# Optimization experiments

Hardware: AMD Instinct MI355X
Metric: run time of the kernel (lower is better)

## Reference

```python
import jax, jax.numpy as jnp
import numpy as np

B, C, DD, HH, WW = 1, 128, 16, 16, 16
D_STATE, D_CONV, EXPAND = 16, 4, 2
D_INNER = EXPAND * C
DT_RANK = (C + 15) // 16


def setup_inputs():
    key = jax.random.key(0)
    ks = jax.random.split(key, 10)
    def w(k, shape, s=0.02):
        return jax.random.normal(k, shape, dtype=jnp.float32) * s
    return {
        "x": jax.random.normal(ks[0], (B, C, DD, HH, WW), dtype=jnp.float32),
        "ln_w": jnp.ones((C,), jnp.float32),
        "ln_b": jnp.zeros((C,), jnp.float32),
        "mnorm_w": jnp.ones((C,), jnp.float32),
        "mnorm_b": jnp.zeros((C,), jnp.float32),
        "in_proj_w": w(ks[1], (2 * D_INNER, C)),
        "conv_w": w(ks[2], (D_INNER, D_CONV), 0.2),
        "conv_b": jnp.zeros((D_INNER,), jnp.float32),
        "x_proj_w": w(ks[3], (DT_RANK + 2 * D_STATE, D_INNER)),
        "dt_proj_w": w(ks[4], (D_INNER, DT_RANK), 0.1),
        "dt_proj_b": jnp.full((D_INNER,), float(np.log(np.expm1(0.01))), jnp.float32),
        "A_log": jnp.log(jnp.tile(jnp.arange(1, D_STATE + 1, dtype=jnp.float32), (D_INNER, 1))),
        "D_param": jnp.ones((D_INNER,), jnp.float32),
        "out_proj_w": w(ks[5], (C, D_INNER)),
        "proj_w": w(ks[6], (C, 3 * C)),
        "proj_b": jnp.zeros((C,), jnp.float32),
        "fc1_w": w(ks[7], (4 * C, C)),
        "fc1_b": jnp.zeros((4 * C,), jnp.float32),
        "fc2_w": w(ks[8], (C, 4 * C)),
        "fc2_b": jnp.zeros((C,), jnp.float32),
    }


def _ln_cf(x, w, b, eps=1e-6):
    # channels_first LayerNorm over axis 1 (matches custom LayerNorm)
    u = x.mean(1, keepdims=True)
    s = ((x - u) ** 2).mean(1, keepdims=True)
    xn = (x - u) * jax.lax.rsqrt(s + eps)
    return w[None, :, None, None, None] * xn + b[None, :, None, None, None]


def _ln_last(x, w, b, eps=1e-5):
    u = x.mean(-1, keepdims=True)
    s = ((x - u) ** 2).mean(-1, keepdims=True)
    return (x - u) * jax.lax.rsqrt(s + eps) * w + b


def _selective_scan(u, delta, A, Bm, Cm, Dv):
    # u, delta: (N,L,d); Bm,Cm: (N,L,n); A: (d,n); Dv: (d,)
    dA = jnp.exp(delta[..., None] * A)                               # (N,L,d,n)
    dBu = delta[..., None] * Bm[:, :, None, :] * u[..., None]         # (N,L,d,n)
    def step(h, inp):
        dA_t, dBu_t, C_t = inp
        h = dA_t * h + dBu_t
        y = jnp.einsum("bdn,bn->bd", h, C_t)
        return h, y
    h0 = jnp.zeros((u.shape[0], A.shape[0], A.shape[1]), u.dtype)
    _, ys = jax.lax.scan(step, h0, (dA.swapaxes(0, 1), dBu.swapaxes(0, 1), Cm.swapaxes(0, 1)))
    return ys.swapaxes(0, 1) + u * Dv


def _mamba(xin, in_proj_w, conv_w, conv_b, x_proj_w, dt_proj_w, dt_proj_b, A_log, D_param, out_proj_w):
    # xin: (N, L, C)
    N, L, _ = xin.shape
    xz = xin @ in_proj_w.T                                            # (N,L,2*d_inner)
    xr, z = jnp.split(xz, 2, axis=-1)
    # causal depthwise conv1d, kernel D_CONV, left-padded (mamba conv1d[..., :L])
    xp = jnp.pad(xr, ((0, 0), (D_CONV - 1, 0), (0, 0)))
    xc = sum(conv_w[:, k] * xp[:, k:k + L, :] for k in range(D_CONV)) + conv_b
    xc = jax.nn.silu(xc)
    x_dbl = xc @ x_proj_w.T                                           # (N,L,dt_rank+2n)
    dt = x_dbl[..., :DT_RANK]
    Bm = x_dbl[..., DT_RANK:DT_RANK + D_STATE]
    Cm = x_dbl[..., DT_RANK + D_STATE:]
    delta = jax.nn.softplus(dt @ dt_proj_w.T + dt_proj_b)
    A = -jnp.exp(A_log)
    y = _selective_scan(xc, delta, A, Bm, Cm, D_param)
    y = y * jax.nn.silu(z)
    return y @ out_proj_w.T


def _forward(x, ln_w, ln_b, mnorm_w, mnorm_b, in_proj_w, conv_w, conv_b, x_proj_w, dt_proj_w, dt_proj_b, A_log, D_param, out_proj_w, proj_w, proj_b, fc1_w, fc1_b, fc2_w, fc2_b):
    Bb, Cc, Dd, Hh, Ww = x.shape
    L = Dd * Hh * Ww
    x1 = _ln_cf(x, ln_w, ln_b)
    # three directional flattenings (d-, h-, w-major); cube => shapes identical
    xd = x1.reshape(Bb, Cc, L)
    xh = x1.transpose(0, 1, 3, 4, 2).reshape(Bb, Cc, L)
    xw = x1.transpose(0, 1, 4, 2, 3).reshape(Bb, Cc, L)
    seq = jnp.stack([xd, xh, xw], 0).reshape(3 * Bb, Cc, L).swapaxes(1, 2)  # (3B,L,C)
    seq = _ln_last(seq, mnorm_w, mnorm_b)
    y = _mamba(seq, in_proj_w, conv_w, conv_b, x_proj_w, dt_proj_w, dt_proj_b, A_log, D_param, out_proj_w)
    # reassemble per-direction volumes (no inverse permute, matching torch code) and concat on channels
    cat = y.swapaxes(1, 2).reshape(3, Bb, Cc, Dd, Hh, Ww).transpose(1, 0, 2, 3, 4, 5).reshape(Bb, 3 * Cc, Dd, Hh, Ww)
    out1 = jnp.einsum("bkdhw,ok->bodhw", cat, proj_w) + proj_b[None, :, None, None, None]
    out_res = x + out1
    h = _ln_cf(out_res, ln_w, ln_b)
    h = jnp.einsum("bcdhw,oc->bodhw", h, fc1_w) + fc1_b[None, :, None, None, None]
    h = jax.nn.gelu(h, approximate=False)
    h = jnp.einsum("bcdhw,oc->bodhw", h, fc2_w) + fc2_b[None, :, None, None, None]
    return h + out_res


def reference(x, ln_w, ln_b, mnorm_w, mnorm_b, in_proj_w, conv_w, conv_b, x_proj_w, dt_proj_w, dt_proj_b, A_log, D_param, out_proj_w, proj_w, proj_b, fc1_w, fc1_b, fc2_w, fc2_b):
    return _forward(x, ln_w, ln_b, mnorm_w, mnorm_b, in_proj_w, conv_w, conv_b, x_proj_w, dt_proj_w, dt_proj_b, A_log, D_param, out_proj_w, proj_w, proj_b, fc1_w, fc1_b, fc2_w, fc2_b)
```

## Files before the change

### kernel.cpp

```cpp
#include <hip/hip_runtime.h>
#include <hip/hip_bf16.h>
#include <math.h>

#define L 4096
#define C 128
#define DI 256
#define NST 16
#define NS 3
#define NCH 256
#define CT 16
#define R3 12288

__device__ __forceinline__ float siluf(float x){ return x / (1.f + __expf(-x)); }
__device__ __forceinline__ float geluf(float x){ return 0.5f*x*(1.f + erff(x*0.70710678118654752f)); }

__device__ __forceinline__ int permf(int s, int l){
  if(s==0) return l;
  if(s==1) return ((l&15)<<8) | ((l>>8)<<4) | ((l>>4)&15);
  return (((l>>4)&15)<<8) | ((l&15)<<4) | (l>>8);
}

__global__ void k_M(const float* __restrict__ opw, const float* __restrict__ pw,
                    float* __restrict__ Mw){
  int b = blockIdx.x;
  int o = b & 127, s = b >> 7;
  int d = threadIdx.x;
  float acc = 0.f;
  for(int c=0;c<C;c++) acc += opw[c*DI + d] * pw[o*384 + s*128 + c];
  Mw[(s*256+d)*128 + o] = acc;
}

__global__ void k_lngemm(const float* __restrict__ x, const float* __restrict__ lw,
                         const float* __restrict__ lb, const float* __restrict__ mw,
                         const float* __restrict__ mb, const float* __restrict__ ipw,
                         float* __restrict__ Z){
  __shared__ float As[128][68];
  __shared__ float Bs[64][132];
  int p0 = blockIdx.x*64, j0 = blockIdx.y*64;
  int tid = threadIdx.x;
  for(int q=0;q<8;q++){
    int f = q*1024 + tid*4; int cc = f>>6, p = f&63;
    float4 v = *(const float4*)&x[cc*L + p0 + p];
    *(float4*)&As[cc][p] = v;
  }
  for(int q=0;q<8;q++){
    int f = q*1024 + tid*4; int j = f>>7, k = f&127;
    float4 b = *(const float4*)&ipw[(j0+j)*C + k];
    *(float4*)&Bs[j][k] = b;
  }
  __syncthreads();
  {
    int p = tid>>2, kg = tid&3;
    float s=0.f, sq=0.f;
    #pragma unroll
    for(int i=0;i<32;i++){
      int k = kg*32 + ((i + kg*2)&31);
      float v = As[k][p]; s += v; sq += v*v;
    }
    s  += __shfl_xor(s,1);  s  += __shfl_xor(s,2);
    sq += __shfl_xor(sq,1); sq += __shfl_xor(sq,2);
    float m1 = s*(1.f/C);
    float r1 = rsqrtf(sq*(1.f/C) - m1*m1 + 1e-6f);
    float s2=0.f, sq2=0.f;
    #pragma unroll
    for(int i=0;i<32;i++){
      int k = kg*32 + ((i + kg*2)&31);
      float t = lw[k]*((As[k][p]-m1)*r1) + lb[k];
      s2 += t; sq2 += t*t;
    }
    s2  += __shfl_xor(s2,1);  s2  += __shfl_xor(s2,2);
    sq2 += __shfl_xor(sq2,1); sq2 += __shfl_xor(sq2,2);
    float m2 = s2*(1.f/C);
    float r2 = rsqrtf(sq2*(1.f/C) - m2*m2 + 1e-5f);
    #pragma unroll
    for(int i=0;i<32;i++){
      int k = kg*32 + ((i + kg*2)&31);
      float t = lw[k]*((As[k][p]-m1)*r1) + lb[k];
      As[k][p] = mw[k]*((t-m2)*r2) + mb[k];
    }
  }
  __syncthreads();
  int og = tid & 15, r4 = tid >> 4;
  float acc[4][4] = {};
  for(int k=0;k<128;k++){
    float4 av = *(const float4*)&As[k][r4*4];
    float a[4] = {av.x, av.y, av.z, av.w};
    float b[4];
    #pragma unroll
    for(int j=0;j<4;j++) b[j] = Bs[og+16*j][k];
    #pragma unroll
    for(int i=0;i<4;i++)
      #pragma unroll
      for(int j=0;j<4;j++) acc[i][j] += a[i]*b[j];
  }
  #pragma unroll
  for(int i=0;i<4;i++)
    #pragma unroll
    for(int j=0;j<4;j++)
      Z[(p0+r4*4+i)*512 + j0 + og + 16*j] = acc[i][j];
}

__global__ void k_conv(const float* __restrict__ Z, const float* __restrict__ cw,
                       const float* __restrict__ cb, float* __restrict__ xc){
  int bl = blockIdx.x;
  int s = bl >> 12, l = bl & 4095;
  int d = threadIdx.x;
  float acc = cb[d];
  #pragma unroll
  for(int k=0;k<4;k++){
    int lk = l - 3 + k;
    if(lk >= 0){
      int p = permf(s, lk);
      acc += cw[d*4+k] * Z[p*512 + d];
    }
  }
  xc[bl*DI + d] = siluf(acc);
}

__global__ void k_xd4a(const float* __restrict__ xc, const float* __restrict__ xpw,
                       float* __restrict__ xp){
  __shared__ float As[32][132];
  __shared__ float Ws[40][132];
  int r0 = blockIdx.x*32;
  int k0 = blockIdx.y*128;
  int tid = threadIdx.x;
  for(int q=0;q<4;q++){
    int f = q*256 + tid; int r = f>>5, kk = (f&31)*4;
    float4 v = *(const float4*)&xc[(r0+r)*DI + k0 + kk];
    *(float4*)&As[r][kk] = v;
  }
  for(int q=0;q<5;q++){
    int f = q*256 + tid; int col = f>>5, kk = (f&31)*4;
    float4 v = *(const float4*)&xpw[col*DI + k0 + kk];
    *(float4*)&Ws[col][kk] = v;
  }
  __syncthreads();
  int r = tid & 31, cg = tid >> 5;
  float acc[5] = {0.f,0.f,0.f,0.f,0.f};
  for(int k4=0;k4<32;k4++){
    float4 a = *(const float4*)&As[r][k4*4];
    #pragma unroll
    for(int j=0;j<5;j++){
      float4 w = *(const float4*)&Ws[cg*5+j][k4*4];
      acc[j] += a.x*w.x + a.y*w.y + a.z*w.z + a.w*w.w;
    }
  }
  float* dst = xp + (blockIdx.y*12288 + r0 + r)*40 + cg*5;
  #pragma unroll
  for(int j=0;j<5;j++) dst[j] = acc[j];
}

__global__ void k_xd4b(const float* __restrict__ xp, const float* __restrict__ dtw,
                       const float* __restrict__ dtb, float* __restrict__ Bc,
                       float* __restrict__ Cc, float* __restrict__ delta){
  __shared__ float xdb[40][17];
  int r0 = blockIdx.x*16;
  int tid = threadIdx.x;
  for(int e=tid; e<640; e+=256){
    int row = e/40, col = e%40;
    int idx = (r0+row)*40 + col;
    xdb[col][row] = xp[idx] + xp[491520 + idx];
  }
  __syncthreads();
  {
    float4 ww0 = *(const float4*)&dtw[tid*8];
    float4 ww1 = *(const float4*)&dtw[tid*8+4];
    float bb = dtb[tid];
    #pragma unroll 4
    for(int r=0;r<16;r++){
      float aa = bb + xdb[0][r]*ww0.x + xdb[1][r]*ww0.y + xdb[2][r]*ww0.z + xdb[3][r]*ww0.w
                    + xdb[4][r]*ww1.x + xdb[5][r]*ww1.y + xdb[6][r]*ww1.z + xdb[7][r]*ww1.w;
      delta[(r0+r)*DI + tid] = (aa > 20.f) ? aa : log1pf(__expf(aa));
    }
  }
  if(tid < 64){
    int rr = tid>>2, ng = (tid&3)*4;
    float4 bv = make_float4(xdb[8+ng][rr], xdb[9+ng][rr], xdb[10+ng][rr], xdb[11+ng][rr]);
    *(float4*)&Bc[(r0+rr)*NST + ng] = bv;
  } else if(tid < 128){
    int t2 = tid - 64;
    int rr = t2>>2, ng = (t2&3)*4;
    float4 cv = make_float4(xdb[24+ng][rr], xdb[25+ng][rr], xdb[26+ng][rr], xdb[27+ng][rr]);
    *(float4*)&Cc[(r0+rr)*NST + ng] = cv;
  }
}

__global__ void k_scanA(const float* __restrict__ delta, const float* __restrict__ xc,
                        const float* __restrict__ Bc, const float* __restrict__ A_log,
                        float* __restrict__ aggA, float* __restrict__ aggB){
  int b = blockIdx.x;
  int ng = b & 3, ch = (b>>2)&255, s = b>>10;
  int d = threadIdx.x;
  int n0 = ng*4;
  float Aa[4], P[4] = {1.f,1.f,1.f,1.f}, S[4] = {0.f,0.f,0.f,0.f};
  #pragma unroll
  for(int j=0;j<4;j++) Aa[j] = -__expf(A_log[d*NST + n0 + j]);
  int base = s*L + ch*CT;
  #pragma unroll
  for(int st=0; st<CT; st++){
    int row = base + st;
    float dl = delta[row*DI + d];
    float u  = xc[row*DI + d];
    float4 bv = *(const float4*)&Bc[row*NST + n0];
    float dlu = dl*u;
    float a;
    a = __expf(dl*Aa[0]); S[0] = a*S[0] + dlu*bv.x; P[0] *= a;
    a = __expf(dl*Aa[1]); S[1] = a*S[1] + dlu*bv.y; P[1] *= a;
    a = __expf(dl*Aa[2]); S[2] = a*S[2] + dlu*bv.z; P[2] *= a;
    a = __expf(dl*Aa[3]); S[3] = a*S[3] + dlu*bv.w; P[3] *= a;
  }
  int idx0 = ch*R3 + s*256 + d;
  #pragma unroll
  for(int j=0;j<4;j++){
    int idx = idx0 + (n0+j)*768;
    aggA[idx] = P[j]; aggB[idx] = S[j];
  }
}

__global__ void k_scanB(const float* __restrict__ aggA, const float* __restrict__ aggB,
                        float* __restrict__ hIn){
  __shared__ float PA[32][9], PB[32][9];
  int tid = threadIdx.x;
  int jl = tid & 31, seg = tid >> 5;
  int j = blockIdx.x*32 + jl;
  int c0 = seg*32;
  float pa[32], pb[32];
  float P = 1.f, S = 0.f;
  #pragma unroll
  for(int i=0;i<32;i++){
    pa[i] = P; pb[i] = S;
    float a = aggA[(c0+i)*R3 + j], b = aggB[(c0+i)*R3 + j];
    S = a*S + b; P = a*P;
  }
  PA[jl][seg] = P; PB[jl][seg] = S;
  __syncthreads();
  if(tid < 32){
    float h = 0.f;
    #pragma unroll
    for(int sg=0; sg<8; sg++){
      float p = PA[tid][sg], s2 = PB[tid][sg];
      PA[tid][sg] = h;
      h = p*h + s2;
    }
  }
  __syncthreads();
  float h0 = PA[jl][seg];
  #pragma unroll
  for(int i=0;i<32;i++){
    hIn[(c0+i)*R3 + j] = pa[i]*h0 + pb[i];
  }
}

__global__ void k_scanC(const float* __restrict__ delta, const float* __restrict__ xc,
                        const float* __restrict__ Bc, const float* __restrict__ Cc,
                        const float* __restrict__ A_log, const float* __restrict__ Dp,
                        const float* __restrict__ Z, const float* __restrict__ hIn,
                        float* __restrict__ yz){
  int b = blockIdx.x;
  int ch = b & 255, s = b >> 8;
  int d = threadIdx.x;
  float Aa[16], h[16];
  #pragma unroll
  for(int n=0;n<16;n++) Aa[n] = -__expf(A_log[d*NST + n]);
  #pragma unroll
  for(int n=0;n<16;n++) h[n] = hIn[ch*R3 + n*768 + s*256 + d];
  float Dv = Dp[d];
  int base = s*L + ch*CT;
  #pragma unroll 2
  for(int st=0; st<CT; st++){
    int row = base + st;
    float dl = delta[row*DI + d];
    float u  = xc[row*DI + d];
    float dlu = dl*u;
    const float4* Bp = (const float4*)&Bc[row*NST];
    const float4* Cp = (const float4*)&Cc[row*NST];
    float y = u*Dv;
    #pragma unroll
    for(int q=0;q<4;q++){
      float4 bv = Bp[q], cv = Cp[q];
      float a;
      a = __expf(dl*Aa[4*q+0]); h[4*q+0] = a*h[4*q+0] + dlu*bv.x; y += h[4*q+0]*cv.x;
      a = __expf(dl*Aa[4*q+1]); h[4*q+1] = a*h[4*q+1] + dlu*bv.y; y += h[4*q+1]*cv.y;
      a = __expf(dl*Aa[4*q+2]); h[4*q+2] = a*h[4*q+2] + dlu*bv.z; y += h[4*q+2]*cv.z;
      a = __expf(dl*Aa[4*q+3]); h[4*q+3] = a*h[4*q+3] + dlu*bv.w; y += h[4*q+3]*cv.w;
    }
    int l = ch*CT + st;
    int p = permf(s, l);
    float zv = Z[p*512 + 256 + d];
    yz[(s*L + l)*DI + d] = y * siluf(zv);
  }
}

__global__ void k_proj(const float* __restrict__ yz, const float* __restrict__ Mw,
                       float* __restrict__ pp){
  __shared__ float As[64][68];
  __shared__ float Bs[64][132];
  int p0 = blockIdx.x*64; int kc = blockIdx.y;
  int s = kc >> 1, d0 = (kc & 1)*128;
  int tid = threadIdx.x;
  int og = tid & 15, r4 = tid >> 4;
  float acc[4][8] = {};
  for(int kk=0; kk<2; kk++){
    int kb = d0 + kk*64;
    for(int q=0;q<4;q++){
      int f = q*1024 + tid*4; int r = f>>6, k = f&63;
      float4 a = *(const float4*)&yz[(s*L + p0 + r)*DI + kb + k];
      *(float4*)&As[r][k] = a;
    }
    for(int q=0;q<8;q++){
      int f = q*1024 + tid*4; int k = f>>7, o = f&127;
      float4 b = *(const float4*)&Mw[(s*256 + kb + k)*128 + o];
      *(float4*)&Bs[k][o] = b;
    }
    __syncthreads();
    for(int k=0;k<64;k++){
      float a[4];
      #pragma unroll
      for(int i=0;i<4;i++) a[i] = As[r4*4+i][k];
      #pragma unroll
      for(int j=0;j<8;j++){
        float bb = Bs[k][og+16*j];
        #pragma unroll
        for(int i=0;i<4;i++) acc[i][j] += a[i]*bb;
      }
    }
    __syncthreads();
  }
  float* dst = pp + kc*524288;
  #pragma unroll
  for(int i=0;i<4;i++)
    #pragma unroll
    for(int j=0;j<8;j++)
      dst[(p0+r4*4+i)*C + og + 16*j] = acc[i][j];
}

__global__ void k_pred(const float* __restrict__ pp, const float* __restrict__ x,
                       const float* __restrict__ pb, float* __restrict__ ores){
  __shared__ float Xs[16][129];
  int p0 = blockIdx.x*16; int tid = threadIdx.x;
  for(int q=0;q<8;q++){
    int f = q*256 + tid; int pl = f&15, o = f>>4;
    Xs[pl][o] = x[o*L + p0 + pl];
  }
  __syncthreads();
  for(int q=0;q<8;q++){
    int f = q*256 + tid; int o = f&127, pl = f>>7;
    int idx = (p0+pl)*C + o;
    float v = pp[idx] + pp[524288+idx] + pp[1048576+idx]
            + pp[1572864+idx] + pp[2097152+idx] + pp[2621440+idx];
    ores[idx] = v + Xs[pl][o] + pb[o];
  }
}

__global__ void k_fc1(const float* __restrict__ ores, const float* __restrict__ lw,
                      const float* __restrict__ lb, const float* __restrict__ w1,
                      const float* __restrict__ b1, float* __restrict__ H){
  __shared__ float As[64][129];
  __shared__ float Bs[64][129];
  int p0 = blockIdx.x*64, j0 = blockIdx.y*64;
  int tid = threadIdx.x;
  for(int q=0;q<8;q++){
    int f = q*1024 + tid*4; int r = f>>7, k = f&127;
    float4 a = *(const float4*)&ores[(p0+r)*C + k];
    As[r][k]=a.x; As[r][k+1]=a.y; As[r][k+2]=a.z; As[r][k+3]=a.w;
    float4 b = *(const float4*)&w1[(j0+r)*C + k];
    Bs[r][k]=b.x; Bs[r][k+1]=b.y; Bs[r][k+2]=b.z; Bs[r][k+3]=b.w;
  }
  __syncthreads();
  {
    int r = tid>>2, kg = tid&3;
    float s=0.f, sq=0.f;
    #pragma unroll
    for(int i=0;i<32;i++){
      int k = kg*32 + ((i + kg*8)&31);
      float v = As[r][k]; s += v; sq += v*v;
    }
    s  += __shfl_xor(s,1);  s  += __shfl_xor(s,2);
    sq += __shfl_xor(sq,1); sq += __shfl_xor(sq,2);
    float m1 = s*(1.f/C);
    float r1 = rsqrtf(sq*(1.f/C) - m1*m1 + 1e-6f);
    #pragma unroll
    for(int i=0;i<32;i++){
      int k = kg*32 + ((i + kg*8)&31);
      As[r][k] = lw[k]*((As[r][k]-m1)*r1) + lb[k];
    }
  }
  __syncthreads();
  int og = tid & 15, r4 = tid >> 4;
  float acc[4][4] = {};
  for(int k=0;k<128;k++){
    float a[4], b[4];
    #pragma unroll
    for(int i=0;i<4;i++) a[i] = As[r4*4+i][k];
    #pragma unroll
    for(int j=0;j<4;j++) b[j] = Bs[og+16*j][k];
    #pragma unroll
    for(int i=0;i<4;i++)
      #pragma unroll
      for(int j=0;j<4;j++) acc[i][j] += a[i]*b[j];
  }
  #pragma unroll
  for(int i=0;i<4;i++)
    #pragma unroll
    for(int j=0;j<4;j++){
      int jj = j0 + og + 16*j;
      H[(p0+r4*4+i)*512 + jj] = geluf(acc[i][j] + b1[jj]);
    }
}

__global__ void k_fc2(const float* __restrict__ H, const float* __restrict__ w2,
                      float* __restrict__ fp){
  __shared__ float As[64][68];
  __shared__ float Bs[128][68];
  int p0 = blockIdx.x*64; int kc = blockIdx.y;
  int tid = threadIdx.x;
  int og = tid & 15, r4 = tid >> 4;
  float acc[4][8] = {};
  for(int kk=0; kk<2; kk++){
    int kb = kc*128 + kk*64;
    for(int q=0;q<4;q++){
      int f = q*1024 + tid*4; int r = f>>6, k = f&63;
      float4 a = *(const float4*)&H[(p0+r)*512 + kb + k];
      *(float4*)&As[r][k] = a;
    }
    for(int q=0;q<8;q++){
      int f = q*1024 + tid*4; int o = f>>6, k = f&63;
      float4 b = *(const float4*)&w2[o*512 + kb + k];
      *(float4*)&Bs[o][k] = b;
    }
    __syncthreads();
    for(int k=0;k<64;k++){
      float a[4];
      #pragma unroll
      for(int i=0;i<4;i++) a[i] = As[r4*4+i][k];
      #pragma unroll
      for(int j=0;j<8;j++){
        float bb = Bs[og+16*j][k];
        #pragma unroll
        for(int i=0;i<4;i++) acc[i][j] += a[i]*bb;
      }
    }
    __syncthreads();
  }
  float* dst = fp + kc*524288;
  #pragma unroll
  for(int i=0;i<4;i++)
    #pragma unroll
    for(int j=0;j<8;j++)
      dst[(p0+r4*4+i)*C + og + 16*j] = acc[i][j];
}

__global__ void k_fred(const float* __restrict__ fp, const float* __restrict__ b2,
                       const float* __restrict__ ores, float* __restrict__ out){
  __shared__ float S[128][17];
  int p0 = blockIdx.x*16; int tid = threadIdx.x;
  for(int q=0;q<8;q++){
    int f = q*256 + tid; int o = f&127, pl = f>>7;
    int idx = (p0+pl)*C + o;
    float v = fp[idx] + fp[524288+idx] + fp[1048576+idx] + fp[1572864+idx];
    S[o][pl] = v + b2[o] + ores[idx];
  }
  __syncthreads();
  for(int q=0;q<8;q++){
    int f = q*256 + tid; int pl = f&15, o = f>>4;
    out[o*L + p0 + pl] = S[o][pl];
  }
}

extern "C" void kernel_launch(void* const* d_in, const int* in_sizes, int n_in,
                              void* d_out, int out_size, void* d_ws, size_t ws_size,
                              hipStream_t stream) {
  const float* x     = (const float*)d_in[0];
  const float* ln_w  = (const float*)d_in[1];
  const float* ln_b  = (const float*)d_in[2];
  const float* mw    = (const float*)d_in[3];
  const float* mb    = (const float*)d_in[4];
  const float* ipw   = (const float*)d_in[5];
  const float* cw    = (const float*)d_in[6];
  const float* cb    = (const float*)d_in[7];
  const float* xpw   = (const float*)d_in[8];
  const float* dtw   = (const float*)d_in[9];
  const float* dtb   = (const float*)d_in[10];
  const float* A_log = (const float*)d_in[11];
  const float* Dp    = (const float*)d_in[12];
  const float* opw   = (const float*)d_in[13];
  const float* pw    = (const float*)d_in[14];
  const float* pb    = (const float*)d_in[15];
  const float* w1    = (const float*)d_in[16];
  const float* b1    = (const float*)d_in[17];
  const float* w2    = (const float*)d_in[18];
  const float* b2    = (const float*)d_in[19];
  float* out = (float*)d_out;

  float* ws = (float*)d_ws;
  float* Z     = ws;
  float* xc    = Z     + 2097152;
  float* delta = xc    + 3145728;
  float* dt    = delta + 3145728;
  float* Bc    = dt    + 98304;
  float* Cc    = Bc    + 196608;
  float* aggA  = Cc    + 196608;
  float* aggB  = aggA  + 3145728;
  float* hIn   = aggB  + 3145728;
  float* Mw    = hIn   + 3145728;
  float* ores  = Mw    + 98304;
  (void)dt;
  float* xp = hIn;
  float* yz = aggA;
  float* pp = delta;
  float* H  = Z;
  float* fp = xc;

  k_M     <<<384, 256, 0, stream>>>(opw, pw, Mw);
  k_lngemm<<<dim3(64,8), 256, 0, stream>>>(x, ln_w, ln_b, mw, mb, ipw, Z);
  k_conv  <<<NS*L, 256, 0, stream>>>(Z, cw, cb, xc);
  k_xd4a  <<<dim3(384,2), 256, 0, stream>>>(xc, xpw, xp);
  k_xd4b  <<<768, 256, 0, stream>>>(xp, dtw, dtb, Bc, Cc, delta);
  k_scanA <<<3072, 256, 0, stream>>>(delta, xc, Bc, A_log, aggA, aggB);
  k_scanB <<<384, 256, 0, stream>>>(aggA, aggB, hIn);
  k_scanC <<<768, 256, 0, stream>>>(delta, xc, Bc, Cc, A_log, Dp, Z, hIn, yz);
  k_proj  <<<dim3(64,6), 256, 0, stream>>>(yz, Mw, pp);
  k_pred  <<<256, 256, 0, stream>>>(pp, x, pb, ores);
  k_fc1   <<<dim3(64,8), 256, 0, stream>>>(ores, ln_w, ln_b, w1, b1, H);
  k_fc2   <<<dim3(64,4), 256, 0, stream>>>(H, w2, fp);
  k_fred  <<<256, 256, 0, stream>>>(fp, b2, ores, out);
}
```

Baseline: 274.3 us.

## Store large intermediate activations in bf16 to halve memory traffic

Converts the big workspace intermediates (Z, xc, delta, scan aggregates, hidden states, yz, partial projection sums, fc1 output, fc2 partials) from fp32 to bf16 storage, with fp32 arithmetic inside kernels. Conversions are round-to-nearest-even bit manipulations, and the workspace layout is rebuilt with byte offsets. This targets the memory-bound pipeline of thirteen kernels, where most time is spent moving these tensors. It costs precision, especially in the scan aggregates and hidden-state carries, which can compound error across the sequence.

```diff
diff --git a/kernel.cpp b/kernel.cpp
--- a/kernel.cpp
+++ b/kernel.cpp
@@ -11,8 +11,20 @@
 #define CT 16
 #define R3 12288
 
+typedef unsigned short u16;
+
 __device__ __forceinline__ float siluf(float x){ return x / (1.f + __expf(-x)); }
 __device__ __forceinline__ float geluf(float x){ return 0.5f*x*(1.f + erff(x*0.70710678118654752f)); }
+
+__device__ __forceinline__ float b2f(u16 h){ return __uint_as_float(((unsigned)h)<<16); }
+__device__ __forceinline__ u16 f2b(float f){
+  unsigned u = __float_as_uint(f);
+  return (u16)((u + 0x7FFFu + ((u>>16)&1u)) >> 16);
+}
+__device__ __forceinline__ float4 b4f(const u16* p){
+  ushort4 v = *(const ushort4*)p;
+  return make_float4(b2f(v.x), b2f(v.y), b2f(v.z), b2f(v.w));
+}
 
 __device__ __forceinline__ int permf(int s, int l){
   if(s==0) return l;
@@ -33,7 +45,7 @@
 __global__ void k_lngemm(const float* __restrict__ x, const float* __restrict__ lw,
                          const float* __restrict__ lb, const float* __restrict__ mw,
                          const float* __restrict__ mb, const float* __restrict__ ipw,
-                         float* __restrict__ Z){
+                         u16* __restrict__ Zb){
   __shared__ float As[128][68];
   __shared__ float Bs[64][132];
   int p0 = blockIdx.x*64, j0 = blockIdx.y*64;
@@ -97,11 +109,11 @@
   for(int i=0;i<4;i++)
     #pragma unroll
     for(int j=0;j<4;j++)
-      Z[(p0+r4*4+i)*512 + j0 + og + 16*j] = acc[i][j];
-}
-
-__global__ void k_conv(const float* __restrict__ Z, const float* __restrict__ cw,
-                       const float* __restrict__ cb, float* __restrict__ xc){
+      Zb[(p0+r4*4+i)*512 + j0 + og + 16*j] = f2b(acc[i][j]);
+}
+
+__global__ void k_conv(const u16* __restrict__ Zb, const float* __restrict__ cw,
+                       const float* __restrict__ cb, u16* __restrict__ xcb){
   int bl = blockIdx.x;
   int s = bl >> 12, l = bl & 4095;
   int d = threadIdx.x;
@@ -111,13 +123,13 @@
     int lk = l - 3 + k;
     if(lk >= 0){
       int p = permf(s, lk);
-      acc += cw[d*4+k] * Z[p*512 + d];
-    }
-  }
-  xc[bl*DI + d] = siluf(acc);
-}
-
-__global__ void k_xd4a(const float* __restrict__ xc, const float* __restrict__ xpw,
+      acc += cw[d*4+k] * b2f(Zb[p*512 + d]);
+    }
+  }
+  xcb[bl*DI + d] = f2b(siluf(acc));
+}
+
+__global__ void k_xd4a(const u16* __restrict__ xcb, const float* __restrict__ xpw,
                        float* __restrict__ xp){
   __shared__ float As[32][132];
   __shared__ float Ws[40][132];
@@ -126,7 +138,7 @@
   int tid = threadIdx.x;
   for(int q=0;q<4;q++){
     int f = q*256 + tid; int r = f>>5, kk = (f&31)*4;
-    float4 v = *(const float4*)&xc[(r0+r)*DI + k0 + kk];
+    float4 v = b4f(&xcb[(r0+r)*DI + k0 + kk]);
     *(float4*)&As[r][kk] = v;
   }
   for(int q=0;q<5;q++){
@@ -152,7 +164,7 @@
 
 __global__ void k_xd4b(const float* __restrict__ xp, const float* __restrict__ dtw,
                        const float* __restrict__ dtb, float* __restrict__ Bc,
-                       float* __restrict__ Cc, float* __restrict__ delta){
+                       float* __restrict__ Cc, u16* __restrict__ deltab){
   __shared__ float xdb[40][17];
   int r0 = blockIdx.x*16;
   int tid = threadIdx.x;
@@ -170,7 +182,8 @@
     for(int r=0;r<16;r++){
       float aa = bb + xdb[0][r]*ww0.x + xdb[1][r]*ww0.y + xdb[2][r]*ww0.z + xdb[3][r]*ww0.w
                     + xdb[4][r]*ww1.x + xdb[5][r]*ww1.y + xdb[6][r]*ww1.z + xdb[7][r]*ww1.w;
-      delta[(r0+r)*DI + tid] = (aa > 20.f) ? aa : log1pf(__expf(aa));
+      float dl = (aa > 20.f) ? aa : log1pf(__expf(aa));
+      deltab[(r0+r)*DI + tid] = f2b(dl);
     }
   }
   if(tid < 64){
@@ -185,9 +198,9 @@
   }
 }
 
-__global__ void k_scanA(const float* __restrict__ delta, const float* __restrict__ xc,
+__global__ void k_scanA(const u16* __restrict__ deltab, const u16* __restrict__ xcb,
                         const float* __restrict__ Bc, const float* __restrict__ A_log,
-                        float* __restrict__ aggA, float* __restrict__ aggB){
+                        u16* __restrict__ aggAb, u16* __restrict__ aggBb){
   int b = blockIdx.x;
   int ng = b & 3, ch = (b>>2)&255, s = b>>10;
   int d = threadIdx.x;
@@ -199,8 +212,8 @@
   #pragma unroll
   for(int st=0; st<CT; st++){
     int row = base + st;
-    float dl = delta[row*DI + d];
-    float u  = xc[row*DI + d];
+    float dl = b2f(deltab[row*DI + d]);
+    float u  = b2f(xcb[row*DI + d]);
     float4 bv = *(const float4*)&Bc[row*NST + n0];
     float dlu = dl*u;
     float a;
@@ -213,12 +226,12 @@
   #pragma unroll
   for(int j=0;j<4;j++){
     int idx = idx0 + (n0+j)*768;
-    aggA[idx] = P[j]; aggB[idx] = S[j];
-  }
-}
-
-__global__ void k_scanB(const float* __restrict__ aggA, const float* __restrict__ aggB,
-                        float* __restrict__ hIn){
+    aggAb[idx] = f2b(P[j]); aggBb[idx] = f2b(S[j]);
+  }
+}
+
+__global__ void k_scanB(const u16* __restrict__ aggAb, const u16* __restrict__ aggBb,
+                        u16* __restrict__ hInb){
   __shared__ float PA[32][9], PB[32][9];
   int tid = threadIdx.x;
   int jl = tid & 31, seg = tid >> 5;
@@ -229,7 +242,7 @@
   #pragma unroll
   for(int i=0;i<32;i++){
     pa[i] = P; pb[i] = S;
-    float a = aggA[(c0+i)*R3 + j], b = aggB[(c0+i)*R3 + j];
+    float a = b2f(aggAb[(c0+i)*R3 + j]), b = b2f(aggBb[(c0+i)*R3 + j]);
     S = a*S + b; P = a*P;
   }
   PA[jl][seg] = P; PB[jl][seg] = S;
@@ -247,15 +260,15 @@
   float h0 = PA[jl][seg];
   #pragma unroll
   for(int i=0;i<32;i++){
-    hIn[(c0+i)*R3 + j] = pa[i]*h0 + pb[i];
-  }
-}
-
-__global__ void k_scanC(const float* __restrict__ delta, const float* __restrict__ xc,
+    hInb[(c0+i)*R3 + j] = f2b(pa[i]*h0 + pb[i]);
+  }
+}
+
+__global__ void k_scanC(const u16* __restrict__ deltab, const u16* __restrict__ xcb,
                         const float* __restrict__ Bc, const float* __restrict__ Cc,
                         const float* __restrict__ A_log, const float* __restrict__ Dp,
-                        const float* __restrict__ Z, const float* __restrict__ hIn,
-                        float* __restrict__ yz){
+                        const u16* __restrict__ Zb, const u16* __restrict__ hInb,
+                        u16* __restrict__ yzb){
   int b = blockIdx.x;
   int ch = b & 255, s = b >> 8;
   int d = threadIdx.x;
@@ -263,14 +276,14 @@
   #pragma unroll
   for(int n=0;n<16;n++) Aa[n] = -__expf(A_log[d*NST + n]);
   #pragma unroll
-  for(int n=0;n<16;n++) h[n] = hIn[ch*R3 + n*768 + s*256 + d];
+  for(int n=0;n<16;n++) h[n] = b2f(hInb[ch*R3 + n*768 + s*256 + d]);
   float Dv = Dp[d];
   int base = s*L + ch*CT;
   #pragma unroll 2
   for(int st=0; st<CT; st++){
     int row = base + st;
-    float dl = delta[row*DI + d];
-    float u  = xc[row*DI + d];
+    float dl = b2f(deltab[row*DI + d]);
+    float u  = b2f(xcb[row*DI + d]);
     float dlu = dl*u;
     const float4* Bp = (const float4*)&Bc[row*NST];
     const float4* Cp = (const float4*)&Cc[row*NST];
@@ -286,13 +299,13 @@
     }
     int l = ch*CT + st;
     int p = permf(s, l);
-    float zv = Z[p*512 + 256 + d];
-    yz[(s*L + l)*DI + d] = y * siluf(zv);
-  }
-}
-
-__global__ void k_proj(const float* __restrict__ yz, const float* __restrict__ Mw,
-                       float* __restrict__ pp){
+    float zv = b2f(Zb[p*512 + 256 + d]);
+    yzb[(s*L + l)*DI + d] = f2b(y * siluf(zv));
+  }
+}
+
+__global__ void k_proj(const u16* __restrict__ yzb, const float* __restrict__ Mw,
+                       u16* __restrict__ ppb){
   __shared__ float As[64][68];
   __shared__ float Bs[64][132];
   int p0 = blockIdx.x*64; int kc = blockIdx.y;
@@ -303,8 +316,8 @@
   for(int kk=0; kk<2; kk++){
     int kb = d0 + kk*64;
     for(int q=0;q<4;q++){
-      int f = q*1024 + tid*4; int r = f>>6, k = f&63;
-      float4 a = *(const float4*)&yz[(s*L + p0 + r)*DI + kb + k];
+      int f = q*256 + tid; int r = f>>4, k = (f&15)*4;
+      float4 a = b4f(&yzb[(s*L + p0 + r)*DI + kb + k]);
       *(float4*)&As[r][k] = a;
     }
     for(int q=0;q<8;q++){
@@ -326,15 +339,15 @@
     }
     __syncthreads();
   }
-  float* dst = pp + kc*524288;
+  u16* dst = ppb + kc*524288;
   #pragma unroll
   for(int i=0;i<4;i++)
     #pragma unroll
     for(int j=0;j<8;j++)
-      dst[(p0+r4*4+i)*C + og + 16*j] = acc[i][j];
-}
-
-__global__ void k_pred(const float* __restrict__ pp, const float* __restrict__ x,
+      dst[(p0+r4*4+i)*C + og + 16*j] = f2b(acc[i][j]);
+}
+
+__global__ void k_pred(const u16* __restrict__ ppb, const float* __restrict__ x,
                        const float* __restrict__ pb, float* __restrict__ ores){
   __shared__ float Xs[16][129];
   int p0 = blockIdx.x*16; int tid = threadIdx.x;
@@ -346,15 +359,15 @@
   for(int q=0;q<8;q++){
     int f = q*256 + tid; int o = f&127, pl = f>>7;
     int idx = (p0+pl)*C + o;
-    float v = pp[idx] + pp[524288+idx] + pp[1048576+idx]
-            + pp[1572864+idx] + pp[2097152+idx] + pp[2621440+idx];
+    float v = b2f(ppb[idx]) + b2f(ppb[524288+idx]) + b2f(ppb[1048576+idx])
+            + b2f(ppb[1572864+idx]) + b2f(ppb[2097152+idx]) + b2f(ppb[2621440+idx]);
     ores[idx] = v + Xs[pl][o] + pb[o];
   }
 }
 
 __global__ void k_fc1(const float* __restrict__ ores, const float* __restrict__ lw,
                       const float* __restrict__ lb, const float* __restrict__ w1,
-                      const float* __restrict__ b1, float* __restrict__ H){
+                      const float* __restrict__ b1, u16* __restrict__ Hb){
   __shared__ float As[64][129];
   __shared__ float Bs[64][129];
   int p0 = blockIdx.x*64, j0 = blockIdx.y*64;
@@ -404,12 +417,12 @@
     #pragma unroll
     for(int j=0;j<4;j++){
       int jj = j0 + og + 16*j;
-      H[(p0+r4*4+i)*512 + jj] = geluf(acc[i][j] + b1[jj]);
-    }
-}
-
-__global__ void k_fc2(const float* __restrict__ H, const float* __restrict__ w2,
-                      float* __restrict__ fp){
+      Hb[(p0+r4*4+i)*512 + jj] = f2b(geluf(acc[i][j] + b1[jj]));
+    }
+}
+
+__global__ void k_fc2(const u16* __restrict__ Hb, const float* __restrict__ w2,
+                      u16* __restrict__ fpb){
   __shared__ float As[64][68];
   __shared__ float Bs[128][68];
   int p0 = blockIdx.x*64; int kc = blockIdx.y;
@@ -419,8 +432,8 @@
   for(int kk=0; kk<2; kk++){
     int kb = kc*128 + kk*64;
     for(int q=0;q<4;q++){
-      int f = q*1024 + tid*4; int r = f>>6, k = f&63;
-      float4 a = *(const float4*)&H[(p0+r)*512 + kb + k];
+      int f = q*256 + tid; int r = f>>4, k = (f&15)*4;
+      float4 a = b4f(&Hb[(p0+r)*512 + kb + k]);
       *(float4*)&As[r][k] = a;
     }
     for(int q=0;q<8;q++){
@@ -442,22 +455,22 @@
     }
     __syncthreads();
   }
-  float* dst = fp + kc*524288;
+  u16* dst = fpb + kc*524288;
   #pragma unroll
   for(int i=0;i<4;i++)
     #pragma unroll
     for(int j=0;j<8;j++)
-      dst[(p0+r4*4+i)*C + og + 16*j] = acc[i][j];
-}
-
-__global__ void k_fred(const float* __restrict__ fp, const float* __restrict__ b2,
+      dst[(p0+r4*4+i)*C + og + 16*j] = f2b(acc[i][j]);
+}
+
+__global__ void k_fred(const u16* __restrict__ fpb, const float* __restrict__ b2,
                        const float* __restrict__ ores, float* __restrict__ out){
   __shared__ float S[128][17];
   int p0 = blockIdx.x*16; int tid = threadIdx.x;
   for(int q=0;q<8;q++){
     int f = q*256 + tid; int o = f&127, pl = f>>7;
     int idx = (p0+pl)*C + o;
-    float v = fp[idx] + fp[524288+idx] + fp[1048576+idx] + fp[1572864+idx];
+    float v = b2f(fpb[idx]) + b2f(fpb[524288+idx]) + b2f(fpb[1048576+idx]) + b2f(fpb[1572864+idx]);
     S[o][pl] = v + b2[o] + ores[idx];
   }
   __syncthreads();
@@ -492,36 +505,34 @@
   const float* b2    = (const float*)d_in[19];
   float* out = (float*)d_out;
 
-  float* ws = (float*)d_ws;
-  float* Z     = ws;
-  float* xc    = Z     + 2097152;
-  float* delta = xc    + 3145728;
-  float* dt    = delta + 3145728;
-  float* Bc    = dt    + 98304;
-  float* Cc    = Bc    + 196608;
-  float* aggA  = Cc    + 196608;
-  float* aggB  = aggA  + 3145728;
-  float* hIn   = aggB  + 3145728;
-  float* Mw    = hIn   + 3145728;
-  float* ores  = Mw    + 98304;
-  (void)dt;
-  float* xp = hIn;
-  float* yz = aggA;
-  float* pp = delta;
-  float* H  = Z;
-  float* fp = xc;
+  char* wsb = (char*)d_ws;
+  u16* Zb     = (u16*)(wsb);
+  u16* xcb    = (u16*)(wsb +  4194304);
+  u16* deltab = (u16*)(wsb + 10485760);
+  u16* aggAb  = (u16*)(wsb + 16777216);
+  u16* aggBb  = (u16*)(wsb + 23068672);
+  u16* hInb   = (u16*)(wsb + 29360128);
+  float* Bc   = (float*)(wsb + 35651584);
+  float* Cc   = (float*)(wsb + 36438016);
+  float* Mw   = (float*)(wsb + 37224448);
+  float* ores = (float*)(wsb + 37617664);
+  float* xp   = (float*)(wsb + 39714816);
+  u16* yzb = aggAb;
+  u16* ppb = deltab;
+  u16* Hb  = Zb;
+  u16* fpb = xcb;
 
   k_M     <<<384, 256, 0, stream>>>(opw, pw, Mw);
-  k_lngemm<<<dim3(64,8), 256, 0, stream>>>(x, ln_w, ln_b, mw, mb, ipw, Z);
-  k_conv  <<<NS*L, 256, 0, stream>>>(Z, cw, cb, xc);
-  k_xd4a  <<<dim3(384,2), 256, 0, stream>>>(xc, xpw, xp);
-  k_xd4b  <<<768, 256, 0, stream>>>(xp, dtw, dtb, Bc, Cc, delta);
-  k_scanA <<<3072, 256, 0, stream>>>(delta, xc, Bc, A_log, aggA, aggB);
-  k_scanB <<<384, 256, 0, stream>>>(aggA, aggB, hIn);
-  k_scanC <<<768, 256, 0, stream>>>(delta, xc, Bc, Cc, A_log, Dp, Z, hIn, yz);
-  k_proj  <<<dim3(64,6), 256, 0, stream>>>(yz, Mw, pp);
-  k_pred  <<<256, 256, 0, stream>>>(pp, x, pb, ores);
-  k_fc1   <<<dim3(64,8), 256, 0, stream>>>(ores, ln_w, ln_b, w1, b1, H);
-  k_fc2   <<<dim3(64,4), 256, 0, stream>>>(H, w2, fp);
-  k_fred  <<<256, 256, 0, stream>>>(fp, b2, ores, out);
-}
+  k_lngemm<<<dim3(64,8), 256, 0, stream>>>(x, ln_w, ln_b, mw, mb, ipw, Zb);
+  k_conv  <<<NS*L, 256, 0, stream>>>(Zb, cw, cb, xcb);
+  k_xd4a  <<<dim3(384,2), 256, 0, stream>>>(xcb, xpw, xp);
+  k_xd4b  <<<768, 256, 0, stream>>>(xp, dtw, dtb, Bc, Cc, deltab);
+  k_scanA <<<3072, 256, 0, stream>>>(deltab, xcb, Bc, A_log, aggAb, aggBb);
+  k_scanB <<<384, 256, 0, stream>>>(aggAb, aggBb, hInb);
+  k_scanC <<<768, 256, 0, stream>>>(deltab, xcb, Bc, Cc, A_log, Dp, Zb, hInb, yzb);
+  k_proj  <<<dim3(64,6), 256, 0, stream>>>(yzb, Mw, ppb);
+  k_pred  <<<256, 256, 0, stream>>>(ppb, x, pb, ores);
+  k_fc1   <<<dim3(64,8), 256, 0, stream>>>(ores, ln_w, ln_b, w1, b1, Hb);
+  k_fc2   <<<dim3(64,4), 256, 0, stream>>>(Hb, w2, fpb);
+  k_fred  <<<256, 256, 0, stream>>>(fpb, b2, ores, out);
+}
```

Result: faster. 255.6 us (-6.8%).
